# Optimization experiments

Measured on AMD Instinct MI355X. Metric: run time of the kernel, lower is better.

## Reference

```python
import jax, jax.numpy as jnp
import numpy as np


def setup_inputs() -> dict:
    key = jax.random.key(0)
    ks = jax.random.split(key, 5)
    B, T, I, H = 64, 2048, 128, 128
    bound = 1.0 / np.sqrt(H)
    x = jax.random.normal(ks[0], (B, T, I), dtype=jnp.float32)
    W_xh = jax.random.uniform(ks[1], (H, I), minval=-bound, maxval=bound, dtype=jnp.float32)
    b_xh = jax.random.uniform(ks[2], (H,), minval=-bound, maxval=bound, dtype=jnp.float32)
    W_hh = jax.random.uniform(ks[3], (H, H), minval=-bound, maxval=bound, dtype=jnp.float32)
    b_hh = jax.random.uniform(ks[4], (H,), minval=-bound, maxval=bound, dtype=jnp.float32)
    return {"x": x, "W_xh": W_xh, "b_xh": b_xh, "W_hh": W_hh, "b_hh": b_hh}


def reference(x, W_xh, b_xh, W_hh, b_hh):
    # x: [B, T, I]; nn.Linear applies x @ W.T + b.
    # Precompute the input projection for all timesteps in one GEMM.
    xp = jnp.einsum('bti,hi->bth', x, W_xh) + b_xh  # [B, T, H]
    B = x.shape[0]
    H = W_hh.shape[0]
    h0 = jnp.zeros((B, H), dtype=x.dtype)

    def step(h, xt):
        h_new = jnp.tanh(xt + h @ W_hh.T + b_hh)
        return h_new, h_new

    h_last, hs = jax.lax.scan(step, h0, jnp.swapaxes(xp, 0, 1))  # hs: [T, B, H]
    h_seq = jnp.swapaxes(hs, 0, 1)  # [B, T, H]
    return h_seq, h_last[None]  # h: [1, B, H]
```

## Files before the change

### kernel.cpp

```cpp
#include <hip/hip_runtime.h>

#define B_ 64
#define T_ 2048
#define I_ 128
#define H_ 128

__global__ __launch_bounds__(256) void xp_gemm(
    const float* __restrict__ x, const float* __restrict__ Wxh,
    const float* __restrict__ bxh, float* __restrict__ xp)
{
    __shared__ float ws[H_ * I_];
    const int tid = threadIdx.x;
    {
        const float4* src = (const float4*)Wxh;
        float4* dst = (float4*)ws;
        #pragma unroll
        for (int i = 0; i < (H_ * I_ / 4) / 256; ++i)
            dst[tid + i * 256] = src[tid + i * 256];
    }
    __syncthreads();

    const int r  = tid & 127;
    const int ch = tid >> 7;
    const long row = (long)blockIdx.x * 128 + r;
    const float* xrow = x + row * I_;
    const float* wb = ws + ch * 64 * I_;

    float acc[64];
    #pragma unroll
    for (int c = 0; c < 64; ++c) acc[c] = 0.f;

    for (int k4 = 0; k4 < I_ / 4; ++k4) {
        const float4 xv = *(const float4*)(xrow + k4 * 4);
        #pragma unroll
        for (int c = 0; c < 64; ++c) {
            const float4 wv = *(const float4*)(wb + c * I_ + k4 * 4);
            acc[c] = fmaf(xv.x, wv.x, acc[c]);
            acc[c] = fmaf(xv.y, wv.y, acc[c]);
            acc[c] = fmaf(xv.z, wv.z, acc[c]);
            acc[c] = fmaf(xv.w, wv.w, acc[c]);
        }
    }

    float* orow = xp + row * H_ + ch * 64;
    const float4* bv = (const float4*)(bxh + ch * 64);
    #pragma unroll
    for (int c4 = 0; c4 < 16; ++c4) {
        const float4 b4 = bv[c4];
        float4 o;
        o.x = acc[c4 * 4 + 0] + b4.x;
        o.y = acc[c4 * 4 + 1] + b4.y;
        o.z = acc[c4 * 4 + 2] + b4.z;
        o.w = acc[c4 * 4 + 3] + b4.w;
        *(float4*)(orow + c4 * 4) = o;
    }
}

__global__ __launch_bounds__(256) void rnn_scan(
    const float* __restrict__ Whh, const float* __restrict__ bhh,
    float* seq ,
    float* hlast )
{
    __shared__ float hb[2][H_];
    const int tid  = threadIdx.x;
    const int j    = tid >> 1;
    const int half = tid & 1;
    const int b    = blockIdx.x;

    float w[64];
    {
        const float* wr = Whh + j * H_ + half * 64;
        #pragma unroll
        for (int i4 = 0; i4 < 16; ++i4) {
            const float4 v = *(const float4*)(wr + i4 * 4);
            w[i4 * 4 + 0] = v.x; w[i4 * 4 + 1] = v.y;
            w[i4 * 4 + 2] = v.z; w[i4 * 4 + 3] = v.w;
        }
    }
    const float bj = bhh[j];
    if (tid < H_) hb[0][tid] = 0.f;

    float* xp = seq + (long)b * T_ * H_;
    float xnext = xp[j];
    __syncthreads();

    int cur = 0;
    for (int t = 0; t < T_; ++t) {
        const float xcur = xnext;
        {
            const int tn = (t + 1 < T_) ? (t + 1) : t;
            xnext = xp[(long)tn * H_ + j];
        }
        const float* hc = hb[cur];
        float a0 = 0.f, a1 = 0.f, a2 = 0.f, a3 = 0.f;
        #pragma unroll
        for (int i4 = 0; i4 < 16; ++i4) {
            const float4 hv = *(const float4*)(hc + half * 64 + i4 * 4);
            a0 = fmaf(hv.x, w[i4 * 4 + 0], a0);
            a1 = fmaf(hv.y, w[i4 * 4 + 1], a1);
            a2 = fmaf(hv.z, w[i4 * 4 + 2], a2);
            a3 = fmaf(hv.w, w[i4 * 4 + 3], a3);
        }
        float s = (a0 + a1) + (a2 + a3);
        s += __shfl_xor(s, 1);
        const float pre = xcur + bj + s;
        const float e = exp2f(pre * 2.8853900817779268f);
        const float hnew = 1.f - 2.f * __builtin_amdgcn_rcpf(e + 1.f);
        if (!half) {
            hb[cur ^ 1][j] = hnew;
            xp[(long)t * H_ + j] = hnew;
        }
        __syncthreads();
        cur ^= 1;
    }
    if (!half) hlast[b * H_ + j] = hb[cur][j];
}

extern "C" void kernel_launch(void* const* d_in, const int* in_sizes, int n_in,
                              void* d_out, int out_size, void* d_ws, size_t ws_size,
                              hipStream_t stream)
{
    const float* x   = (const float*)d_in[0];
    const float* Wxh = (const float*)d_in[1];
    const float* bxh = (const float*)d_in[2];
    const float* Whh = (const float*)d_in[3];
    const float* bhh = (const float*)d_in[4];
    float* out   = (float*)d_out;
    float* hlast = out + (size_t)B_ * T_ * H_;

    xp_gemm<<<(B_ * T_) / 128, 256, 0, stream>>>(x, Wxh, bxh, out);
    rnn_scan<<<B_, 256, 0, stream>>>(Whh, bhh, out, hlast);
}
```

Baseline: 1.110 ms.

## Stage xp chunks into LDS asynchronously and use lightweight barrier in RNN scan

The recurrent scan now loads 128-timestep chunks of the precomputed input projection into double-buffered shared memory with global_load_lds, prefetching the next chunk while the current one is processed. This takes the per-step global load latency off the serial recurrence. The per-step __syncthreads is replaced by an lgkmcnt wait plus s_barrier, which avoids waiting on the outstanding global stores and async loads. The hidden-state buffer is padded (136 entries) so the two halves sit in different banks. The trade-off is 128 KB of LDS per block, and correctness depends on the hand-written waitcnt ordering.

```diff
diff --git a/kernel.cpp b/kernel.cpp
--- a/kernel.cpp
+++ b/kernel.cpp
@@ -4,6 +4,8 @@
 #define T_ 2048
 #define I_ 128
 #define H_ 128
+#define CHUNK 128
+#define NCHUNK (T_ / CHUNK)
 
 __global__ __launch_bounds__(256) void xp_gemm(
     const float* __restrict__ x, const float* __restrict__ Wxh,
@@ -56,16 +58,32 @@
     }
 }
 
-__global__ __launch_bounds__(256) void rnn_scan(
+__device__ __forceinline__ void stage_chunk(const float* __restrict__ g,
+                                            float* l, int wv, int ln)
+{
+    #pragma unroll
+    for (int i = 0; i < 16; ++i) {
+        const int off = i * 1024 + wv * 256;
+        __builtin_amdgcn_global_load_lds(
+            (const __attribute__((address_space(1))) unsigned int*)(g + off + ln * 4),
+            (__attribute__((address_space(3))) unsigned int*)(l + off),
+            16, 0, 0);
+    }
+}
+
+__global__ __launch_bounds__(256, 1) void rnn_scan(
     const float* __restrict__ Whh, const float* __restrict__ bhh,
-    float* seq ,
-    float* hlast )
+    float* __restrict__ seq , float* __restrict__ hlast)
 {
-    __shared__ float hb[2][H_];
+    __shared__ float xpl[2][CHUNK * H_];
+    __shared__ float hb[2][136];
+
     const int tid  = threadIdx.x;
     const int j    = tid >> 1;
     const int half = tid & 1;
     const int b    = blockIdx.x;
+    const int wv   = tid >> 6;
+    const int ln   = tid & 63;
 
     float w[64];
     {
@@ -78,42 +96,50 @@
         }
     }
     const float bj = bhh[j];
-    if (tid < H_) hb[0][tid] = 0.f;
+    if (tid < 136) { hb[0][tid] = 0.f; hb[1][tid] = 0.f; }
 
-    float* xp = seq + (long)b * T_ * H_;
-    float xnext = xp[j];
-    __syncthreads();
+    float* xp = seq + (size_t)b * T_ * H_;
 
+    stage_chunk(xp, &xpl[0][0], wv, ln);
+
+    const int slot = j + ((j >> 6) << 2);
     int cur = 0;
-    for (int t = 0; t < T_; ++t) {
-        const float xcur = xnext;
-        {
-            const int tn = (t + 1 < T_) ? (t + 1) : t;
-            xnext = xp[(long)tn * H_ + j];
+    for (int c = 0; c < NCHUNK; ++c) {
+        asm volatile("s_waitcnt vmcnt(0)" ::: "memory");
+        __syncthreads();
+        if (c + 1 < NCHUNK)
+            stage_chunk(xp + (size_t)(c + 1) * CHUNK * H_, &xpl[(c + 1) & 1][0], wv, ln);
+
+        const float* xb = &xpl[c & 1][0];
+        float* sq = xp + (size_t)c * CHUNK * H_;
+
+        for (int t = 0; t < CHUNK; ++t) {
+            const float xcur = xb[t * H_ + j];
+            const float* hc = &hb[cur][half * 68];
+            float a0 = 0.f, a1 = 0.f, a2 = 0.f, a3 = 0.f;
+            #pragma unroll
+            for (int i4 = 0; i4 < 16; ++i4) {
+                const float4 hv = *(const float4*)(hc + i4 * 4);
+                a0 = fmaf(hv.x, w[i4 * 4 + 0], a0);
+                a1 = fmaf(hv.y, w[i4 * 4 + 1], a1);
+                a2 = fmaf(hv.z, w[i4 * 4 + 2], a2);
+                a3 = fmaf(hv.w, w[i4 * 4 + 3], a3);
+            }
+            float s = (a0 + a1) + (a2 + a3);
+            s += __shfl_xor(s, 1);
+            const float pre = xcur + bj + s;
+            const float e = exp2f(pre * 2.8853900817779268f);
+            const float hnew = 1.f - 2.f * __builtin_amdgcn_rcpf(e + 1.f);
+            if (!half) {
+                hb[cur ^ 1][slot] = hnew;
+                sq[t * H_ + j] = hnew;
+            }
+            asm volatile("s_waitcnt lgkmcnt(0)" ::: "memory");
+            __builtin_amdgcn_s_barrier();
+            cur ^= 1;
         }
-        const float* hc = hb[cur];
-        float a0 = 0.f, a1 = 0.f, a2 = 0.f, a3 = 0.f;
-        #pragma unroll
-        for (int i4 = 0; i4 < 16; ++i4) {
-            const float4 hv = *(const float4*)(hc + half * 64 + i4 * 4);
-            a0 = fmaf(hv.x, w[i4 * 4 + 0], a0);
-            a1 = fmaf(hv.y, w[i4 * 4 + 1], a1);
-            a2 = fmaf(hv.z, w[i4 * 4 + 2], a2);
-            a3 = fmaf(hv.w, w[i4 * 4 + 3], a3);
-        }
-        float s = (a0 + a1) + (a2 + a3);
-        s += __shfl_xor(s, 1);
-        const float pre = xcur + bj + s;
-        const float e = exp2f(pre * 2.8853900817779268f);
-        const float hnew = 1.f - 2.f * __builtin_amdgcn_rcpf(e + 1.f);
-        if (!half) {
-            hb[cur ^ 1][j] = hnew;
-            xp[(long)t * H_ + j] = hnew;
-        }
-        __syncthreads();
-        cur ^= 1;
     }
-    if (!half) hlast[b * H_ + j] = hb[cur][j];
+    if (!half) hlast[b * H_ + j] = hb[cur][slot];
 }
 
 extern "C" void kernel_launch(void* const* d_in, const int* in_sizes, int n_in,
```

Result: slower. 1.172 ms (+5.6%).
